# Kernel tuning notes

Measured on AMD Instinct MI355X. Metric: run time of the kernel, lower is better.

## Reference

```python
import jax, jax.numpy as jnp
import numpy as np

B, N, K = 2, 8192, 9
FEAT_C, COST_C, FLOW_C = 128, 64, 3
CH = [128, 128]          # PointConv output channels
MLP = [128, 64]          # pointwise Conv1d channels
WN = 16                  # WeightNet output width
HID = [8, 8]             # WeightNet hidden widths
SLOPE = 0.1              # leaky relu slope
EPS = 1e-5
CLAMP = (-200.0, 200.0)


def setup_inputs() -> dict:
    key = jax.random.key(0)
    ks = iter(jax.random.split(key, 64))
    def nrm(shape, s=0.02):
        return jax.random.normal(next(ks), shape, jnp.float32) * s
    inp = {}
    inp["xyz"] = jax.random.normal(next(ks), (B, N, 3), jnp.float32)
    inp["feats"] = jax.random.normal(next(ks), (B, FEAT_C, N), jnp.float32)
    inp["cost_volume"] = jax.random.normal(next(ks), (B, COST_C, N), jnp.float32)
    inp["flow"] = jax.random.normal(next(ks), (B, FLOW_C, N), jnp.float32)
    last = FEAT_C + COST_C + FLOW_C
    for i, co in enumerate(CH):
        cin = last + 3
        p = f"pc{i}_"
        inp[p + "w1"] = nrm((HID[0], 3)); inp[p + "b1"] = jnp.zeros((HID[0],), jnp.float32)
        inp[p + "w2"] = nrm((HID[1], HID[0])); inp[p + "b2"] = jnp.zeros((HID[1],), jnp.float32)
        inp[p + "w3"] = nrm((WN, HID[1])); inp[p + "b3"] = jnp.zeros((WN,), jnp.float32)
        inp[p + "linW"] = nrm((co, cin * WN)); inp[p + "linb"] = jnp.zeros((co,), jnp.float32)
        last = co
    for i, co in enumerate(MLP):
        inp[f"mlp{i}_W"] = nrm((co, last)); inp[f"mlp{i}_b"] = jnp.zeros((co,), jnp.float32)
        last = co
    inp["fc_W"] = nrm((3, last)); inp["fc_b"] = jnp.zeros((3,), jnp.float32)
    return inp


def _bn(x, axes):
    m = x.mean(axes, keepdims=True)
    v = x.var(axes, keepdims=True)
    return (x - m) / jnp.sqrt(v + EPS)


def _leaky(x):
    return jnp.where(x >= 0, x, SLOPE * x)


def _knn_idx(xyz, k):
    # xyz: [B,N,3] -> idx [B,N,K] of k nearest (incl. self)
    sq = jnp.sum(xyz * xyz, -1)                       # [B,N]
    d = sq[:, :, None] + sq[:, None, :] - 2.0 * jnp.einsum('bnc,bmc->bnm', xyz, xyz)
    return jax.lax.top_k(-d, k)[1]                    # [B,N,K]


def _gather(a, idx):
    # a: [B,N,C], idx: [B,N,K] -> [B,N,K,C]
    return jax.vmap(lambda x, i: x[i])(a, idx)


def _pointconv(xyz, points, idx, w1, b1, w2, b2, w3, b3, linW, linb):
    # xyz [B,N,3], points [B,C,N] -> [B,out,N]
    g_xyz = _gather(xyz, idx) - xyz[:, :, None, :]    # [B,N,K,3] relative coords
    g_pts = _gather(jnp.transpose(points, (0, 2, 1)), idx)  # [B,N,K,C]
    grouped = jnp.concatenate([g_pts, g_xyz], -1)     # [B,N,K,C+3]
    # WeightNet on relative coords: 3 -> 8 -> 8 -> 16 (bn+relu each)
    h = jax.nn.relu(_bn(g_xyz @ w1.T + b1, (0, 1, 2)))
    h = jax.nn.relu(_bn(h @ w2.T + b2, (0, 1, 2)))
    w = jax.nn.relu(_bn(h @ w3.T + b3, (0, 1, 2)))    # [B,N,K,WN]
    bsz, n = grouped.shape[0], grouped.shape[1]
    agg = jnp.einsum('bnkc,bnkw->bncw', grouped, w).reshape(bsz, n, -1)
    out = agg @ linW.T + linb                         # [B,N,out]
    out = _leaky(_bn(out, (0, 1)))
    return jnp.transpose(out, (0, 2, 1))              # [B,out,N]


def reference(xyz, feats, cost_volume, flow,
              pc0_w1, pc0_b1, pc0_w2, pc0_b2, pc0_w3, pc0_b3, pc0_linW, pc0_linb,
              pc1_w1, pc1_b1, pc1_w2, pc1_b2, pc1_w3, pc1_b3, pc1_linW, pc1_linb,
              mlp0_W, mlp0_b, mlp1_W, mlp1_b, fc_W, fc_b):
    idx = _knn_idx(xyz, K)
    x = jnp.concatenate([feats, cost_volume, flow], axis=1)  # [B, feat+cost+flow, N]
    x = _pointconv(xyz, x, idx, pc0_w1, pc0_b1, pc0_w2, pc0_b2, pc0_w3, pc0_b3, pc0_linW, pc0_linb)
    x = _pointconv(xyz, x, idx, pc1_w1, pc1_b1, pc1_w2, pc1_b2, pc1_w3, pc1_b3, pc1_linW, pc1_linb)
    x = _leaky(jnp.einsum('oc,bcn->bon', mlp0_W, x) + mlp0_b[None, :, None])
    x = _leaky(jnp.einsum('oc,bcn->bon', mlp1_W, x) + mlp1_b[None, :, None])
    fl = jnp.einsum('oc,bcn->bon', fc_W, x) + fc_b[None, :, None]
    return x, jnp.clip(fl, CLAMP[0], CLAMP[1])
```

## Files before the change

### kernel.cpp

```cpp
#include <hip/hip_runtime.h>

#define NBATCH 2
#define NPTS   8192
#define NPT    (NBATCH*NPTS)
#define KNN    9
#define SEG    16
#define SEGN   (NPTS/SEG)
#define SCAP   16
#define SSTR   17

typedef unsigned short u16;
typedef unsigned int   u32;
typedef short bf16x8 __attribute__((ext_vector_type(8)));
typedef float f32x4  __attribute__((ext_vector_type(4)));

__device__ __forceinline__ float wred(float v){
#pragma unroll
  for(int o=32;o>0;o>>=1) v += __shfl_down(v,o);
  return v;
}

__device__ __forceinline__ u16 f2b(float f){
  u32 u = __float_as_uint(f);
  return (u16)((u + 0x7fffu + ((u>>16)&1u)) >> 16);
}
__device__ __forceinline__ float b2f(u16 h){ return __uint_as_float(((u32)h)<<16); }

__device__ __forceinline__ float bumpup(float x){
  u32 u = __float_as_uint(x);
  if(u == 0x80000000u) u = 1u;
  else if((int)u >= 0) u += 1u;
  else u -= 1u;
  return __uint_as_float(u);
}

__global__ __launch_bounds__(256) void k_build_xin(
    const float* __restrict__ feats, const float* __restrict__ cost,
    const float* __restrict__ flow, float* __restrict__ xin)
{
  __shared__ float buf[196][67];
  int t = threadIdx.x;
  int pt0 = blockIdx.x*64;
  int b = pt0 >> 13, n0 = pt0 & (NPTS-1);
  int lane = t & 63, grp = t >> 6;
  const float* f  = feats + (size_t)b*128*NPTS + n0 + lane;
  const float* cv = cost  + (size_t)b*64 *NPTS + n0 + lane;
  const float* fl = flow  + (size_t)b*3  *NPTS + n0 + lane;
  for(int c=grp; c<128; c+=4) buf[c][lane]      = f[(size_t)c*NPTS];
  for(int c=grp; c<64;  c+=4) buf[128+c][lane]  = cv[(size_t)c*NPTS];
  if(grp<3) buf[192+grp][lane] = fl[(size_t)grp*NPTS];
  else      buf[195][lane] = 0.f;
  __syncthreads();
  for(int e=t; e<64*49; e+=256){
    int p = e/49, q = e-p*49;
    float4 v = make_float4(buf[4*q][p], buf[4*q+1][p], buf[4*q+2][p], buf[4*q+3][p]);
    *(float4*)(xin + (size_t)(pt0+p)*196 + 4*q) = v;
  }
}

__global__ __launch_bounds__(256) void k_thr(
    const float* __restrict__ xyz, float* __restrict__ thr)
{
  __shared__ float md[4][64][9];
  int t = threadIdx.x, lane = t & 63, wave = t >> 6;
  int qb = blockIdx.x;
  int b = qb >> 7;
  int n = (qb & 127)*64 + lane;
  const float* xb = xyz + (size_t)b*NPTS*3;
  float qx=xb[3*n], qy=xb[3*n+1], qz=xb[3*n+2];
  float qs = __fadd_rn(__fadd_rn(__fmul_rn(qx,qx),__fmul_rn(qy,qy)),__fmul_rn(qz,qz));
  float bd[KNN];
#pragma unroll
  for(int i=0;i<KNN;i++) bd[i]=__builtin_inff();
  for(int i=0;i<128;i++){
    int m = (wave*128 + i)*16;
    float cx=xb[3*m], cy=xb[3*m+1], cz=xb[3*m+2];
    float s = __fadd_rn(__fadd_rn(__fmul_rn(cx,cx),__fmul_rn(cy,cy)),__fmul_rn(cz,cz));
    float dot = fmaf(cz,qz, fmaf(cy,qy, __fmul_rn(cx,qx)));
    float d = __fsub_rn(__fadd_rn(qs,s), __fmul_rn(2.0f,dot));
    if(d < bd[KNN-1]){
      bd[KNN-1]=d;
#pragma unroll
      for(int r=KNN-2;r>=0;r--){
        if(bd[r+1] < bd[r]){ float td=bd[r]; bd[r]=bd[r+1]; bd[r+1]=td; }
      }
    }
  }
#pragma unroll
  for(int i=0;i<KNN;i++) md[wave][lane][i]=bd[i];
  __syncthreads();
  if(t < 64){
    float b2[KNN];
#pragma unroll
    for(int i=0;i<KNN;i++) b2[i]=__builtin_inff();
    for(int w=0;w<4;w++){
#pragma unroll
      for(int i=0;i<KNN;i++){
        float d = md[w][t][i];
        if(d < b2[KNN-1]){
          b2[KNN-1]=d;
#pragma unroll
          for(int r=KNN-2;r>=0;r--){
            if(b2[r+1] < b2[r]){ float td=b2[r]; b2[r]=b2[r+1]; b2[r+1]=td; }
          }
        }
      }
    }
    thr[(b<<13) + (qb & 127)*64 + t] = b2[KNN-1];
  }
}

__global__ __launch_bounds__(256) void k_knn_part(
    const float* __restrict__ xyz, const float* __restrict__ thr,
    float* __restrict__ pd, int* __restrict__ pi)
{
  __shared__ float4 cbuf[256];
  __shared__ float sdq[256*SSTR];
  __shared__ int   sqi[256*SSTR];
  int t = threadIdx.x;
  int seg = blockIdx.x & (SEG-1);
  int qc  = blockIdx.x >> 4;
  int b = qc >> 5;
  int n = (qc & 31)*256 + t;
  int pt = (b<<13) + n;
  const float* xb = xyz + (size_t)b*NPTS*3;
  float qx=xb[3*n], qy=xb[3*n+1], qz=xb[3*n+2];
  float qs = __fadd_rn(__fadd_rn(__fmul_rn(qx,qx),__fmul_rn(qy,qy)),__fmul_rn(qz,qz));
  float init = bumpup(thr[pt]);
  float bd[KNN]; int bi[KNN];
#pragma unroll
  for(int i=0;i<KNN;i++){ bd[i]=init; bi[i]=0x7fffffff; }
  float cut = init;
  int cnt = 0;
  float* msd = sdq + t*SSTR;
  int*   msi = sqi + t*SSTR;
  auto flush = [&](){
    for(int i=0;i<cnt;i++){
      float d = msd[i]; int id = msi[i];
      if(d < bd[KNN-1]){
        bd[KNN-1]=d; bi[KNN-1]=id;
#pragma unroll
        for(int r=KNN-2;r>=0;r--){
          if(bd[r+1] < bd[r]){
            float td=bd[r]; bd[r]=bd[r+1]; bd[r+1]=td;
            int ti=bi[r]; bi[r]=bi[r+1]; bi[r+1]=ti;
          }
        }
      }
    }
    cnt = 0;
    cut = bd[KNN-1];
  };
  const int m0 = seg*SEGN;
  for(int tt=0; tt<SEGN; tt+=256){
    int m = m0 + tt + t;
    float cx=xb[3*m], cy=xb[3*m+1], cz=xb[3*m+2];
    float s = __fadd_rn(__fadd_rn(__fmul_rn(cx,cx),__fmul_rn(cy,cy)),__fmul_rn(cz,cz));
    cbuf[t] = make_float4(cx,cy,cz,s);
    __syncthreads();
#pragma unroll 4
    for(int j=0;j<256;j++){
      float4 c = cbuf[j];
      float dot = fmaf(c.z,qz, fmaf(c.y,qy, __fmul_rn(c.x,qx)));
      float d = __fsub_rn(__fadd_rn(qs,c.w), __fmul_rn(2.0f,dot));
      if(d < cut){
        msd[cnt]=d; msi[cnt]=m0+tt+j; cnt++;
        if(cnt==SCAP) flush();
      }
    }
    __syncthreads();
  }
  flush();
  size_t base = ((size_t)pt*SEG + seg)*KNN;
#pragma unroll
  for(int i=0;i<KNN;i++){ pd[base+i]=bd[i]; pi[base+i]=bi[i]; }
}

__global__ __launch_bounds__(256) void k_knn_merge(
    const float* __restrict__ pd, const int* __restrict__ pi, int* __restrict__ idxo)
{
  int pt = blockIdx.x*256 + threadIdx.x;
  const float4* dp = (const float4*)(pd + (size_t)pt*SEG*KNN);
  const int4*   ip = (const int4*)(pi + (size_t)pt*SEG*KNN);
  float bd[KNN]; int bi[KNN];
#pragma unroll
  for(int i=0;i<KNN;i++){ bd[i]=__builtin_inff(); bi[i]=0x7fffffff; }
  for(int v=0; v<SEG*KNN/4; v++){
    float4 dv = dp[v];
    int4   iv = ip[v];
    float dd[4] = {dv.x,dv.y,dv.z,dv.w};
    int   ii[4] = {iv.x,iv.y,iv.z,iv.w};
#pragma unroll
    for(int u=0;u<4;u++){
      float d = dd[u]; int id = ii[u];
      if(d < bd[KNN-1]){
        bd[KNN-1]=d; bi[KNN-1]=id;
#pragma unroll
        for(int i=KNN-2;i>=0;i--){
          if(bd[i+1] < bd[i]){
            float td=bd[i]; bd[i]=bd[i+1]; bd[i+1]=td;
            int ti=bi[i]; bi[i]=bi[i+1]; bi[i+1]=ti;
          }
        }
      }
    }
  }
#pragma unroll
  for(int r=0;r<KNN;r++) idxo[pt*KNN + r] = bi[r];
}

__global__ __launch_bounds__(256) void k_wn1(
    const float* __restrict__ xyz, const int* __restrict__ idx,
    const float* __restrict__ W, const float* __restrict__ Bv,
    float* __restrict__ hout, float* __restrict__ partial)
{
  int t = threadIdx.x;
  int e = blockIdx.x*256 + t;
  int pt = e/KNN;
  int b = pt>>13, n = pt & (NPTS-1);
  int m = idx[e];
  const float* xb = xyz + (size_t)b*NPTS*3;
  float gx = xb[3*m]-xb[3*n], gy = xb[3*m+1]-xb[3*n+1], gz = xb[3*m+2]-xb[3*n+2];
  float v[8];
#pragma unroll
  for(int j=0;j<8;j++){
    float d = fmaf(gz, W[3*j+2], fmaf(gy, W[3*j+1], gx*W[3*j]));
    v[j] = d + Bv[j];
    hout[(size_t)e*8 + j] = v[j];
  }
  __shared__ float red[4][2][8];
  int wave = t>>6, lane = t&63;
#pragma unroll
  for(int j=0;j<8;j++){
    float s = wred(v[j]);
    float q = wred(v[j]*v[j]);
    if(lane==0){ red[wave][0][j]=s; red[wave][1][j]=q; }
  }
  __syncthreads();
  if(t < 16){
    int isq = t>>3, c = t&7;
    partial[blockIdx.x*16 + t] =
      red[0][isq][c]+red[1][isq][c]+red[2][isq][c]+red[3][isq][c];
  }
}

template<int CI, int CO>
__global__ __launch_bounds__(256) void k_wn23(
    const float* __restrict__ hin, const float* __restrict__ st,
    const float* __restrict__ W, const float* __restrict__ Bv,
    float* __restrict__ hout, float* __restrict__ partial)
{
  int t = threadIdx.x;
  int e = blockIdx.x*256 + t;
  float x[CI];
#pragma unroll
  for(int i=0;i<CI;i++){
    float v = (hin[(size_t)e*CI + i] - st[i])*st[CI+i];
    x[i] = v>0.f? v : 0.f;
  }
  float v[CO];
#pragma unroll
  for(int j=0;j<CO;j++){
    float d = 0.f;
#pragma unroll
    for(int i=0;i<CI;i++) d = fmaf(x[i], W[j*CI+i], d);
    v[j] = d + Bv[j];
    hout[(size_t)e*CO + j] = v[j];
  }
  __shared__ float red[4][2][CO];
  int wave = t>>6, lane = t&63;
#pragma unroll
  for(int j=0;j<CO;j++){
    float s = wred(v[j]);
    float q = wred(v[j]*v[j]);
    if(lane==0){ red[wave][0][j]=s; red[wave][1][j]=q; }
  }
  __syncthreads();
  if(t < 2*CO){
    int isq = t/CO, c = t%CO;
    partial[blockIdx.x*2*CO + t] =
      red[0][isq][c]+red[1][isq][c]+red[2][isq][c]+red[3][isq][c];
  }
}

__global__ __launch_bounds__(256) void k_fin(
    const float* __restrict__ partial, float* __restrict__ st,
    int C, int nb, float cnt)
{
  __shared__ float sa[256], qa[256];
  int t = threadIdx.x;
  int c = t % C;
  int r0 = t / C;
  int stride = 256 / C;
  float s=0.f, q=0.f;
  for(int r=r0; r<nb; r+=stride){
    s += partial[r*2*C + c];
    q += partial[r*2*C + C + c];
  }
  sa[t]=s; qa[t]=q;
  __syncthreads();
  if(t < C){
    for(int g=1; g<stride; g++){ s += sa[t+g*C]; q += qa[t+g*C]; }
    float mean = s/cnt;
    float var  = q/cnt - mean*mean;
    st[t]   = mean;
    st[C+t] = 1.0f/sqrtf(var + 1e-5f);
  }
}

__global__ __launch_bounds__(256) void k_prepW(
    const float* __restrict__ linW, u16* __restrict__ Wh, u16* __restrict__ Wl,
    int AW, int KP)
{
  int e = blockIdx.x*256 + threadIdx.x;
  if(e >= 128*KP) return;
  int o = e / KP, k = e - o*KP;
  float w = (k < AW) ? linW[o*AW + k] : 0.f;
  u16 h = f2b(w);
  u16 l = f2b(w - b2f(h));
  Wh[e]=h; Wl[e]=l;
}

template<int CIN, int XSTRIDE, int KP>
__global__ __launch_bounds__(256) void k_buildA(
    const float* __restrict__ xin, const float* __restrict__ xyz,
    const int* __restrict__ idx, const float* __restrict__ wpre,
    const float* __restrict__ st3, u16* __restrict__ Abuf, int c0)
{
  constexpr int P = 8;
  constexpr int CPTS = CIN-3;
  constexpr int CPAD = KP/16;
  __shared__ float wm[P][KNN][16];
  __shared__ float gxs[P][KNN][3];
  __shared__ int   si[P][KNN];
  __shared__ float sm3[16], sr3[16];
  int t = threadIdx.x;
  int pt0 = c0 + blockIdx.x*P;
  int b = pt0 >> 13;
  const float* xb = xyz + (size_t)b*NPTS*3;
  if(t<16){ sm3[t]=st3[t]; sr3[t]=st3[16+t]; }
  if(t>=32 && t<32+P*KNN){
    int u = t-32; int p=u/KNN, k=u-p*KNN;
    int n = (pt0+p)&(NPTS-1);
    int m = idx[(pt0+p)*KNN+k];
    si[p][k]=m;
    gxs[p][k][0]=xb[3*m]  -xb[3*n];
    gxs[p][k][1]=xb[3*m+1]-xb[3*n+1];
    gxs[p][k][2]=xb[3*m+2]-xb[3*n+2];
  }
  __syncthreads();
  for(int e=t; e<P*KNN*16; e+=256){
    int p = e/(KNN*16); int r = e - p*(KNN*16); int k = r>>4, wn = r&15;
    float v = (wpre[((size_t)(pt0+p)*KNN + k)*16 + wn] - sm3[wn]) * sr3[wn];
    wm[p][k][wn] = v>0.f? v:0.f;
  }
  __syncthreads();
  for(int it=t; it<P*CPAD; it+=256){
    int p = it/CPAD, c = it - p*CPAD;
    u32 u[8];
    if(c < CIN){
      float g[KNN];
      if(c < CPTS){
#pragma unroll
        for(int k=0;k<KNN;k++)
          g[k] = xin[(size_t)((b<<13) + si[p][k])*XSTRIDE + c];
      } else {
        int cc = c - CPTS;
#pragma unroll
        for(int k=0;k<KNN;k++) g[k] = gxs[p][k][cc];
      }
      float a[16];
#pragma unroll
      for(int wn=0; wn<16; wn++){
        float s = 0.f;
#pragma unroll
        for(int k=0;k<KNN;k++) s = fmaf(g[k], wm[p][k][wn], s);
        a[wn] = s;
      }
#pragma unroll
      for(int j=0;j<8;j++)
        u[j] = (u32)f2b(a[2*j]) | ((u32)f2b(a[2*j+1])<<16);
    } else {
#pragma unroll
      for(int j=0;j<8;j++) u[j]=0;
    }
    u32* dst = (u32*)(Abuf + ((size_t)(blockIdx.x*P + p)*KP + c*16));
    uint4 v0 = make_uint4(u[0],u[1],u[2],u[3]);
    uint4 v1 = make_uint4(u[4],u[5],u[6],u[7]);
    *(uint4*)dst = v0;
    *((uint4*)dst + 1) = v1;
  }
}

__device__ __forceinline__ void gload16(const void* g, void* l){
  __builtin_amdgcn_global_load_lds(
      (const __attribute__((address_space(1))) u32*)g,
      (__attribute__((address_space(3))) u32*)l, 16, 0, 0);
}

template<int KP>
__global__ __launch_bounds__(256) void k_gemm(
    const u16* __restrict__ Wh, const u16* __restrict__ Wl,
    const u16* __restrict__ A, const float* __restrict__ linb,
    float* __restrict__ outp, int ptBase)
{
  __shared__ __attribute__((aligned(16))) u16 lds[40960];
  constexpr int NT = KP/64;
  int t = threadIdx.x, wave = t>>6, lane = t&63;
  int p0 = blockIdx.x*64;
  const u16* Ab = A + (size_t)p0*KP;

  auto stage = [&](const u16* __restrict__ g, int k0, int ldsByteOff, int rows){
    int nr = (rows*128) >> 12;
    for(int r=0;r<nr;r++){
      int y  = (r*4 + wave) << 10;
      int yl = y + lane*16;
      int row = yl >> 7;
      int s = (yl >> 4) & 7;
      int c = s ^ (row & 7);
      const u16* src = g + (size_t)row*KP + k0 + c*8;
      gload16(src, (char*)lds + ldsByteOff + y);
    }
  };

  stage(Wh, 0, 0,     128);
  stage(Wl, 0, 32768, 128);
  stage(Ab, 0, 65536, 64);

  f32x4 acch[2][4], accl[2][4];
#pragma unroll
  for(int i=0;i<2;i++)
#pragma unroll
    for(int j=0;j<4;j++){ acch[i][j]=(f32x4)(0.f); accl[i][j]=(f32x4)(0.f); }

  for(int kt=0; kt<NT; kt++){
    int cur = kt & 1;
    __syncthreads();
    if(kt+1 < NT){
      int nxt = cur^1;
      stage(Wh, (kt+1)*64, nxt*16384,         128);
      stage(Wl, (kt+1)*64, 32768 + nxt*16384, 128);
      stage(Ab, (kt+1)*64, 65536 + nxt*8192,  64);
    }
    const u16* Lwh = lds + cur*8192;
    const u16* Lwl = lds + 16384 + cur*8192;
    const u16* La  = lds + 32768 + cur*4096;
#pragma unroll
    for(int kf=0; kf<2; kf++){
      int cb = kf*4 + (lane>>4);
      bf16x8 af[4];
#pragma unroll
      for(int nf=0; nf<4; nf++){
        int p = nf*16 + (lane&15);
        af[nf] = *(const bf16x8*)(La + p*64 + ((cb ^ (p&7))<<3));
      }
#pragma unroll
      for(int mf=0; mf<2; mf++){
        int row = (wave*2+mf)*16 + (lane&15);
        int off = row*64 + ((cb ^ (row&7))<<3);
        bf16x8 wh = *(const bf16x8*)(Lwh + off);
        bf16x8 wl = *(const bf16x8*)(Lwl + off);
#pragma unroll
        for(int nf=0; nf<4; nf++){
          acch[mf][nf] = __builtin_amdgcn_mfma_f32_16x16x32_bf16(wh, af[nf], acch[mf][nf], 0,0,0);
          accl[mf][nf] = __builtin_amdgcn_mfma_f32_16x16x32_bf16(wl, af[nf], accl[mf][nf], 0,0,0);
        }
      }
    }
  }
#pragma unroll
  for(int mf=0; mf<2; mf++){
#pragma unroll
    for(int nf=0; nf<4; nf++){
      f32x4 v = acch[mf][nf] + accl[mf][nf];
      int pt = ptBase + p0 + nf*16 + (lane&15);
      int obase = (wave*2+mf)*16 + (lane>>4)*4;
#pragma unroll
      for(int r=0;r<4;r++){
        int o = obase + r;
        outp[(size_t)pt*128 + o] = v[r] + linb[o];
      }
    }
  }
}

__global__ __launch_bounds__(256) void k_ostats(
    const float* __restrict__ outp, float* __restrict__ partial)
{
  __shared__ float ss[256], qq[256];
  int t = threadIdx.x;
  int c = t & 127, half = t >> 7;
  int base_pt = blockIdx.x*256;
  float s=0.f, q=0.f;
  for(int i=0;i<128;i++){
    int pt = base_pt + i*2 + half;
    float v = outp[(size_t)pt*128 + c];
    s += v; q = fmaf(v,v,q);
  }
  ss[t]=s; qq[t]=q;
  __syncthreads();
  if(t<128){
    partial[blockIdx.x*256 + t]       = ss[t]+ss[t+128];
    partial[blockIdx.x*256 + 128 + t] = qq[t]+qq[t+128];
  }
}

__global__ __launch_bounds__(256) void k_pfin(
    const float* __restrict__ outp, const float* __restrict__ st,
    float* __restrict__ xout)
{
  int e = blockIdx.x*256 + threadIdx.x;
  int c = e & 127;
  float v = (outp[e]-st[c])*st[128+c];
  xout[e] = v>=0.f? v : 0.1f*v;
}

__global__ __launch_bounds__(256) void k_mlp(
    const float* __restrict__ x2,
    const float* __restrict__ W0, const float* __restrict__ B0,
    const float* __restrict__ W1, const float* __restrict__ B1,
    const float* __restrict__ Wf, const float* __restrict__ Bf,
    float* __restrict__ dout)
{
  __shared__ float w0l[128*129];
  __shared__ float w1l[128*65];
  __shared__ float xt [128*65];
  __shared__ float m1l[64*65];
  int t = threadIdx.x;
  int pt0 = blockIdx.x*64;
  int b = pt0 >> 13, n0 = pt0 & (NPTS-1);
  for(int e=t; e<128*128; e+=256){ int o=e>>7, j=e&127; w0l[j*129+o] = W0[e]; }
  for(int e=t; e<64*128;  e+=256){ int o=e>>7, j=e&127; w1l[j*65+o]  = W1[e]; }
  for(int e=t; e<64*128;  e+=256){ int p=e>>7, j=e&127; xt[j*65+p]   = x2[(size_t)(pt0+p)*128 + j]; }
  __syncthreads();
  int p = t&63, wv = t>>6;
  float acc[32];
#pragma unroll
  for(int i=0;i<32;i++) acc[i]=0.f;
  for(int j=0;j<128;j++){
    float xv = xt[j*65+p];
#pragma unroll
    for(int i=0;i<32;i++)
      acc[i] = fmaf(w0l[j*129 + wv*32 + i], xv, acc[i]);
  }
  __syncthreads();
#pragma unroll
  for(int i=0;i<32;i++){
    float v = acc[i] + B0[wv*32+i];
    v = v>=0.f? v : 0.1f*v;
    xt[(wv*32+i)*65 + p] = v;
  }
  __syncthreads();
  float a2[16];
#pragma unroll
  for(int i=0;i<16;i++) a2[i]=0.f;
  for(int j=0;j<128;j++){
    float xv = xt[j*65+p];
#pragma unroll
    for(int i=0;i<16;i++)
      a2[i] = fmaf(w1l[j*65 + wv*16 + i], xv, a2[i]);
  }
#pragma unroll
  for(int i=0;i<16;i++){
    int o = wv*16+i;
    float v = a2[i] + B1[o];
    v = v>=0.f? v : 0.1f*v;
    dout[(size_t)(b*64+o)*NPTS + n0 + p] = v;
    m1l[o*65+p] = v;
  }
  __syncthreads();
  if(t < 192){
    int o = t/64, pp = t%64;
    float a = Bf[o];
    for(int j=0;j<64;j++) a = fmaf(Wf[o*64+j], m1l[j*65+pp], a);
    a = fminf(fmaxf(a, -200.f), 200.f);
    dout[(size_t)NBATCH*64*NPTS + (size_t)(b*3+o)*NPTS + n0 + pp] = a;
  }
}

extern "C" void kernel_launch(void* const* d_in, const int* in_sizes, int n_in,
                              void* d_out, int out_size, void* d_ws, size_t ws_size,
                              hipStream_t stream)
{
  (void)in_sizes; (void)n_in; (void)out_size;
  const float* xyz   = (const float*)d_in[0];
  const float* feats = (const float*)d_in[1];
  const float* cost  = (const float*)d_in[2];
  const float* flow  = (const float*)d_in[3];
  const float* pw1[2]  = {(const float*)d_in[4],  (const float*)d_in[12]};
  const float* pb1[2]  = {(const float*)d_in[5],  (const float*)d_in[13]};
  const float* pw2[2]  = {(const float*)d_in[6],  (const float*)d_in[14]};
  const float* pb2[2]  = {(const float*)d_in[7],  (const float*)d_in[15]};
  const float* pw3[2]  = {(const float*)d_in[8],  (const float*)d_in[16]};
  const float* pb3[2]  = {(const float*)d_in[9],  (const float*)d_in[17]};
  const float* plW[2]  = {(const float*)d_in[10], (const float*)d_in[18]};
  const float* plb[2]  = {(const float*)d_in[11], (const float*)d_in[19]};
  const float* m0W = (const float*)d_in[20];
  const float* m0b = (const float*)d_in[21];
  const float* m1W = (const float*)d_in[22];
  const float* m1b = (const float*)d_in[23];
  const float* fcW = (const float*)d_in[24];
  const float* fcb = (const float*)d_in[25];
  float* out = (float*)d_out;

  const int KP0 = 3200, AW0 = 3168;
  const int KP1 = 2112, AW1 = 2096;

  float* ws = (float*)d_ws;
  size_t o = 0;
  float* xin0 = ws + o; o += (size_t)NPT*196;
  int*   idx  = (int*)(ws + o); o += (size_t)NPT*KNN + 3;
  o &= ~(size_t)3;
  float* thr  = ws + o; o += (size_t)NPT;
  float* pd   = ws + o; o += (size_t)NPT*SEG*KNN;
  int*   pi   = (int*)(ws + o); o += (size_t)NPT*SEG*KNN;
  float* h1   = ws + o; o += (size_t)NPT*KNN*8;
  float* h2   = ws + o; o += (size_t)NPT*KNN*8;
  float* wpre = ws + o; o += (size_t)NPT*KNN*16;
  float* part = ws + o; o += 576*32;
  float* st1  = ws + o; o += 16;
  float* st2  = ws + o; o += 16;
  float* st3  = ws + o; o += 32;
  float* sto  = ws + o; o += 256;
  float* outp = ws + o; o += (size_t)NPT*128;
  float* x1   = ws + o; o += (size_t)NPT*128;
  float* x2   = ws + o; o += (size_t)NPT*128;
  u16* Wh0 = (u16*)(ws + o); o += (size_t)128*KP0/2;
  u16* Wl0 = (u16*)(ws + o); o += (size_t)128*KP0/2;
  u16* Wh1 = (u16*)(ws + o); o += (size_t)128*KP1/2;
  u16* Wl1 = (u16*)(ws + o); o += (size_t)128*KP1/2;
  u16* Abuf = (u16*)(ws + o);
  size_t used_bytes = o*4;
  size_t avail = ws_size > used_bytes ? ws_size - used_bytes : 0;
  int npc = NPT;
  while(npc > 1024 && (size_t)npc*KP0*2 > avail) npc >>= 1;

  k_build_xin<<<NPT/64, 256, 0, stream>>>(feats, cost, flow, xin0);
  k_thr<<<256, 256, 0, stream>>>(xyz, thr);
  k_knn_part<<<64*SEG, 256, 0, stream>>>(xyz, thr, pd, pi);
  k_knn_merge<<<NPT/256, 256, 0, stream>>>(pd, pi, idx);

  k_prepW<<<(128*KP0+255)/256, 256, 0, stream>>>(plW[0], Wh0, Wl0, AW0, KP0);
  k_prepW<<<(128*KP1+255)/256, 256, 0, stream>>>(plW[1], Wh1, Wl1, AW1, KP1);

  const float cnt1 = (float)(NPT*KNN);
  const float cnto = (float)NPT;

  for(int L=0; L<2; ++L){
    k_wn1<<<576,256,0,stream>>>(xyz, idx, pw1[L], pb1[L], h1, part);
    k_fin<<<1,256,0,stream>>>(part, st1, 8, 576, cnt1);
    k_wn23<8,8><<<576,256,0,stream>>>(h1, st1, pw2[L], pb2[L], h2, part);
    k_fin<<<1,256,0,stream>>>(part, st2, 8, 576, cnt1);
    k_wn23<8,16><<<576,256,0,stream>>>(h2, st2, pw3[L], pb3[L], wpre, part);
    k_fin<<<1,256,0,stream>>>(part, st3, 16, 576, cnt1);
    for(int c0 = 0; c0 < NPT; c0 += npc){
      if(L==0){
        k_buildA<198,196,KP0><<<npc/8,256,0,stream>>>(xin0, xyz, idx, wpre, st3, Abuf, c0);
        k_gemm<KP0><<<npc/64,256,0,stream>>>(Wh0, Wl0, Abuf, plb[0], outp, c0);
      } else {
        k_buildA<131,128,KP1><<<npc/8,256,0,stream>>>(x1, xyz, idx, wpre, st3, Abuf, c0);
        k_gemm<KP1><<<npc/64,256,0,stream>>>(Wh1, Wl1, Abuf, plb[1], outp, c0);
      }
    }
    k_ostats<<<64,256,0,stream>>>(outp, part);
    k_fin<<<1,256,0,stream>>>(part, sto, 128, 64, cnto);
    k_pfin<<<NPT*128/256,256,0,stream>>>(outp, sto, (L==0)? x1 : x2);
  }

  k_mlp<<<NPT/64,256,0,stream>>>(x2, m0W,m0b, m1W,m1b, fcW,fcb, out);
}
```

Baseline: 561.6 us.

## Fuse PointConv A-matrix build into GEMM, drop split-bf16 weights, fuse output stats

Merges the separate buildA and GEMM kernels into one kernel. Each block gathers the neighbour features, computes the weighted einsum tile in LDS and feeds it straight to the MFMA loop, so the large A buffer never goes through global memory. It also stops splitting the weights into high and low bf16 parts, which halves the MFMA and weight traffic but lowers accuracy. The GEMM epilogue now writes per-block sum and sum-of-squares for the output BN, replacing the ostats kernel. Separately, the KNN selection capacity constants are shrunk.

```diff
diff --git a/kernel.cpp b/kernel.cpp
--- a/kernel.cpp
+++ b/kernel.cpp
@@ -6,8 +6,8 @@
 #define KNN    9
 #define SEG    16
 #define SEGN   (NPTS/SEG)
-#define SCAP   16
-#define SSTR   17
+#define SCAP   12
+#define SSTR   13
 
 typedef unsigned short u16;
 typedef unsigned int   u32;
@@ -24,7 +24,6 @@
   u32 u = __float_as_uint(f);
   return (u16)((u + 0x7fffu + ((u>>16)&1u)) >> 16);
 }
-__device__ __forceinline__ float b2f(u16 h){ return __uint_as_float(((u32)h)<<16); }
 
 __device__ __forceinline__ float bumpup(float x){
   u32 u = __float_as_uint(x);
@@ -309,87 +308,13 @@
 }
 
 __global__ __launch_bounds__(256) void k_prepW(
-    const float* __restrict__ linW, u16* __restrict__ Wh, u16* __restrict__ Wl,
-    int AW, int KP)
+    const float* __restrict__ linW, u16* __restrict__ Wh, int AW, int KP)
 {
   int e = blockIdx.x*256 + threadIdx.x;
   if(e >= 128*KP) return;
   int o = e / KP, k = e - o*KP;
   float w = (k < AW) ? linW[o*AW + k] : 0.f;
-  u16 h = f2b(w);
-  u16 l = f2b(w - b2f(h));
-  Wh[e]=h; Wl[e]=l;
-}
-
-template<int CIN, int XSTRIDE, int KP>
-__global__ __launch_bounds__(256) void k_buildA(
-    const float* __restrict__ xin, const float* __restrict__ xyz,
-    const int* __restrict__ idx, const float* __restrict__ wpre,
-    const float* __restrict__ st3, u16* __restrict__ Abuf, int c0)
-{
-  constexpr int P = 8;
-  constexpr int CPTS = CIN-3;
-  constexpr int CPAD = KP/16;
-  __shared__ float wm[P][KNN][16];
-  __shared__ float gxs[P][KNN][3];
-  __shared__ int   si[P][KNN];
-  __shared__ float sm3[16], sr3[16];
-  int t = threadIdx.x;
-  int pt0 = c0 + blockIdx.x*P;
-  int b = pt0 >> 13;
-  const float* xb = xyz + (size_t)b*NPTS*3;
-  if(t<16){ sm3[t]=st3[t]; sr3[t]=st3[16+t]; }
-  if(t>=32 && t<32+P*KNN){
-    int u = t-32; int p=u/KNN, k=u-p*KNN;
-    int n = (pt0+p)&(NPTS-1);
-    int m = idx[(pt0+p)*KNN+k];
-    si[p][k]=m;
-    gxs[p][k][0]=xb[3*m]  -xb[3*n];
-    gxs[p][k][1]=xb[3*m+1]-xb[3*n+1];
-    gxs[p][k][2]=xb[3*m+2]-xb[3*n+2];
-  }
-  __syncthreads();
-  for(int e=t; e<P*KNN*16; e+=256){
-    int p = e/(KNN*16); int r = e - p*(KNN*16); int k = r>>4, wn = r&15;
-    float v = (wpre[((size_t)(pt0+p)*KNN + k)*16 + wn] - sm3[wn]) * sr3[wn];
-    wm[p][k][wn] = v>0.f? v:0.f;
-  }
-  __syncthreads();
-  for(int it=t; it<P*CPAD; it+=256){
-    int p = it/CPAD, c = it - p*CPAD;
-    u32 u[8];
-    if(c < CIN){
-      float g[KNN];
-      if(c < CPTS){
-#pragma unroll
-        for(int k=0;k<KNN;k++)
-          g[k] = xin[(size_t)((b<<13) + si[p][k])*XSTRIDE + c];
-      } else {
-        int cc = c - CPTS;
-#pragma unroll
-        for(int k=0;k<KNN;k++) g[k] = gxs[p][k][cc];
-      }
-      float a[16];
-#pragma unroll
-      for(int wn=0; wn<16; wn++){
-        float s = 0.f;
-#pragma unroll
-        for(int k=0;k<KNN;k++) s = fmaf(g[k], wm[p][k][wn], s);
-        a[wn] = s;
-      }
-#pragma unroll
-      for(int j=0;j<8;j++)
-        u[j] = (u32)f2b(a[2*j]) | ((u32)f2b(a[2*j+1])<<16);
-    } else {
-#pragma unroll
-      for(int j=0;j<8;j++) u[j]=0;
-    }
-    u32* dst = (u32*)(Abuf + ((size_t)(blockIdx.x*P + p)*KP + c*16));
-    uint4 v0 = make_uint4(u[0],u[1],u[2],u[3]);
-    uint4 v1 = make_uint4(u[4],u[5],u[6],u[7]);
-    *(uint4*)dst = v0;
-    *((uint4*)dst + 1) = v1;
-  }
+  Wh[e] = f2b(w);
 }
 
 __device__ __forceinline__ void gload16(const void* g, void* l){
@@ -398,53 +323,141 @@
       (__attribute__((address_space(3))) u32*)l, 16, 0, 0);
 }
 
-template<int KP>
-__global__ __launch_bounds__(256) void k_gemm(
-    const u16* __restrict__ Wh, const u16* __restrict__ Wl,
-    const u16* __restrict__ A, const float* __restrict__ linb,
-    float* __restrict__ outp, int ptBase)
-{
-  __shared__ __attribute__((aligned(16))) u16 lds[40960];
+template<int CIN, int XSTRIDE, int KP>
+__global__ __launch_bounds__(256) void k_pcgemm(
+    const float* __restrict__ xin, const float* __restrict__ xyz,
+    const int* __restrict__ idx, const float* __restrict__ wpre,
+    const float* __restrict__ st3, const u16* __restrict__ Wh,
+    const float* __restrict__ linb, float* __restrict__ outp,
+    float* __restrict__ partial)
+{
+  constexpr int CPTS = CIN-3;
   constexpr int NT = KP/64;
+  __shared__ __attribute__((aligned(16))) char smem[71680];
+  u16*   Wlds = (u16*)smem;
+  u16*   Alds = (u16*)(smem + 32768);
+  float* G    = (float*)(smem + 49152);
+  float* gxs  = (float*)(smem + 62464);
+  int*   si   = (int*)(smem + 69376);
+
   int t = threadIdx.x, wave = t>>6, lane = t&63;
-  int p0 = blockIdx.x*64;
-  const u16* Ab = A + (size_t)p0*KP;
-
-  auto stage = [&](const u16* __restrict__ g, int k0, int ldsByteOff, int rows){
-    int nr = (rows*128) >> 12;
-    for(int r=0;r<nr;r++){
+  int pt0 = blockIdx.x*64;
+  int b = pt0 >> 13;
+  const float* xb = xyz + (size_t)b*NPTS*3;
+  const float* xbase = xin + ((size_t)(b<<13))*XSTRIDE;
+
+  int p_ = t>>2, wq = t&3;
+
+  for(int e=t; e<64*KNN; e+=256){
+    int p = e/KNN, k = e - p*KNN;
+    int n = (pt0+p)&(NPTS-1);
+    int m = idx[(pt0+p)*KNN+k];
+    si[p*KNN+k] = m;
+    gxs[(p*KNN+k)*3+0] = xb[3*m]  -xb[3*n];
+    gxs[(p*KNN+k)*3+1] = xb[3*m+1]-xb[3*n+1];
+    gxs[(p*KNN+k)*3+2] = xb[3*m+2]-xb[3*n+2];
+  }
+  float wm[KNN][4];
+  {
+    float sm[4], sr[4];
+#pragma unroll
+    for(int j=0;j<4;j++){ sm[j]=st3[wq*4+j]; sr[j]=st3[16+wq*4+j]; }
+#pragma unroll
+    for(int k=0;k<KNN;k++){
+      float4 w4 = *(const float4*)(wpre + ((size_t)(pt0+p_)*KNN + k)*16 + wq*4);
+      float wv[4] = {w4.x,w4.y,w4.z,w4.w};
+#pragma unroll
+      for(int j=0;j<4;j++){
+        float v = (wv[j]-sm[j])*sr[j];
+        wm[k][j] = v>0.f? v:0.f;
+      }
+    }
+  }
+  __syncthreads();
+
+  auto stageW = [&](int kt, int buf){
+    int k0 = kt*64;
+#pragma unroll
+    for(int r=0;r<4;r++){
       int y  = (r*4 + wave) << 10;
       int yl = y + lane*16;
       int row = yl >> 7;
       int s = (yl >> 4) & 7;
       int c = s ^ (row & 7);
-      const u16* src = g + (size_t)row*KP + k0 + c*8;
-      gload16(src, (char*)lds + ldsByteOff + y);
+      const u16* src = Wh + (size_t)row*KP + k0 + c*8;
+      gload16(src, (char*)smem + buf*16384 + y);
     }
   };
 
-  stage(Wh, 0, 0,     128);
-  stage(Wl, 0, 32768, 128);
-  stage(Ab, 0, 65536, 64);
-
-  f32x4 acch[2][4], accl[2][4];
+  auto gatherG = [&](int kt){
+    int c0 = kt*4;
+    for(int e=t; e<64*KNN; e+=256){
+      int p = e/KNN, k = e - p*KNN;
+      float v[4];
+      if(c0+3 < CPTS){
+        float4 f4 = *(const float4*)(xbase + (size_t)si[p*KNN+k]*XSTRIDE + c0);
+        v[0]=f4.x; v[1]=f4.y; v[2]=f4.z; v[3]=f4.w;
+      } else {
+#pragma unroll
+        for(int j=0;j<4;j++){
+          int c = c0+j;
+          if(c < CPTS)      v[j] = xbase[(size_t)si[p*KNN+k]*XSTRIDE + c];
+          else if(c < CIN)  v[j] = gxs[(p*KNN+k)*3 + (c-CPTS)];
+          else              v[j] = 0.f;
+        }
+      }
+#pragma unroll
+      for(int j=0;j<4;j++) G[p*52 + j*12 + k] = v[j];
+    }
+  };
+
+  auto einsumA = [&](int buf){
+    float g[4][KNN];
+#pragma unroll
+    for(int ci=0;ci<4;ci++){
+      const float* gp = G + p_*52 + ci*12;
+      float4 a4 = *(const float4*)(gp);
+      float4 b4 = *(const float4*)(gp+4);
+      g[ci][0]=a4.x; g[ci][1]=a4.y; g[ci][2]=a4.z; g[ci][3]=a4.w;
+      g[ci][4]=b4.x; g[ci][5]=b4.y; g[ci][6]=b4.z; g[ci][7]=b4.w;
+      g[ci][8]=gp[8];
+    }
+#pragma unroll
+    for(int ci=0;ci<4;ci++){
+      float a[4];
+#pragma unroll
+      for(int j=0;j<4;j++){
+        float s = 0.f;
+#pragma unroll
+        for(int k=0;k<KNN;k++) s = fmaf(g[ci][k], wm[k][j], s);
+        a[j] = s;
+      }
+      u32 lo = (u32)f2b(a[0]) | ((u32)f2b(a[1])<<16);
+      u32 hi = (u32)f2b(a[2]) | ((u32)f2b(a[3])<<16);
+      int chunk = ci*2 + (wq>>1);
+      int off = buf*8192 + p_*128 + ((chunk ^ (p_&7))<<4) + (wq&1)*8;
+      *(uint2*)((char*)Alds + off) = make_uint2(lo,hi);
+    }
+  };
+
+  gatherG(0); stageW(0, 0);
+  __syncthreads();
+  einsumA(0);
+  __syncthreads();
+
+  f32x4 acc[2][4];
 #pragma unroll
   for(int i=0;i<2;i++)
 #pragma unroll
-    for(int j=0;j<4;j++){ acch[i][j]=(f32x4)(0.f); accl[i][j]=(f32x4)(0.f); }
+    for(int j=0;j<4;j++) acc[i][j]=(f32x4)(0.f);
 
   for(int kt=0; kt<NT; kt++){
-    int cur = kt & 1;
+    int cur = kt & 1, nxt = cur^1;
+    if(kt+1 < NT){ gatherG(kt+1); stageW(kt+1, nxt); }
     __syncthreads();
-    if(kt+1 < NT){
-      int nxt = cur^1;
-      stage(Wh, (kt+1)*64, nxt*16384,         128);
-      stage(Wl, (kt+1)*64, 32768 + nxt*16384, 128);
-      stage(Ab, (kt+1)*64, 65536 + nxt*8192,  64);
-    }
-    const u16* Lwh = lds + cur*8192;
-    const u16* Lwl = lds + 16384 + cur*8192;
-    const u16* La  = lds + 32768 + cur*4096;
+    if(kt+1 < NT) einsumA(nxt);
+    const u16* Lw = Wlds + cur*8192;
+    const u16* La = Alds + cur*4096;
 #pragma unroll
     for(int kf=0; kf<2; kf++){
       int cb = kf*4 + (lane>>4);
@@ -457,51 +470,40 @@
 #pragma unroll
       for(int mf=0; mf<2; mf++){
         int row = (wave*2+mf)*16 + (lane&15);
-        int off = row*64 + ((cb ^ (row&7))<<3);
-        bf16x8 wh = *(const bf16x8*)(Lwh + off);
-        bf16x8 wl = *(const bf16x8*)(Lwl + off);
-#pragma unroll
-        for(int nf=0; nf<4; nf++){
-          acch[mf][nf] = __builtin_amdgcn_mfma_f32_16x16x32_bf16(wh, af[nf], acch[mf][nf], 0,0,0);
-          accl[mf][nf] = __builtin_amdgcn_mfma_f32_16x16x32_bf16(wl, af[nf], accl[mf][nf], 0,0,0);
-        }
-      }
-    }
-  }
+        bf16x8 wh = *(const bf16x8*)(Lw + row*64 + ((cb ^ (row&7))<<3));
+#pragma unroll
+        for(int nf=0; nf<4; nf++)
+          acc[mf][nf] = __builtin_amdgcn_mfma_f32_16x16x32_bf16(wh, af[nf], acc[mf][nf], 0,0,0);
+      }
+    }
+    __syncthreads();
+  }
+
+  int q = lane>>4, lc = lane&15;
 #pragma unroll
   for(int mf=0; mf<2; mf++){
-#pragma unroll
-    for(int nf=0; nf<4; nf++){
-      f32x4 v = acch[mf][nf] + accl[mf][nf];
-      int pt = ptBase + p0 + nf*16 + (lane&15);
-      int obase = (wave*2+mf)*16 + (lane>>4)*4;
-#pragma unroll
-      for(int r=0;r<4;r++){
-        int o = obase + r;
-        outp[(size_t)pt*128 + o] = v[r] + linb[o];
-      }
-    }
-  }
-}
-
-__global__ __launch_bounds__(256) void k_ostats(
-    const float* __restrict__ outp, float* __restrict__ partial)
-{
-  __shared__ float ss[256], qq[256];
-  int t = threadIdx.x;
-  int c = t & 127, half = t >> 7;
-  int base_pt = blockIdx.x*256;
-  float s=0.f, q=0.f;
-  for(int i=0;i<128;i++){
-    int pt = base_pt + i*2 + half;
-    float v = outp[(size_t)pt*128 + c];
-    s += v; q = fmaf(v,v,q);
-  }
-  ss[t]=s; qq[t]=q;
-  __syncthreads();
-  if(t<128){
-    partial[blockIdx.x*256 + t]       = ss[t]+ss[t+128];
-    partial[blockIdx.x*256 + 128 + t] = qq[t]+qq[t+128];
+    int obase = (wave*2+mf)*16 + q*4;
+#pragma unroll
+    for(int r=0;r<4;r++){
+      int o = obase + r;
+      float bo = linb[o];
+      float sv = 0.f, qv = 0.f;
+#pragma unroll
+      for(int nf=0; nf<4; nf++){
+        float x = acc[mf][nf][r] + bo;
+        outp[(size_t)(pt0 + nf*16 + lc)*128 + o] = x;
+        sv += x; qv = fmaf(x,x,qv);
+      }
+#pragma unroll
+      for(int off=8; off>0; off>>=1){
+        sv += __shfl_down(sv,off);
+        qv += __shfl_down(qv,off);
+      }
+      if(lc==0){
+        partial[blockIdx.x*256 + o]       = sv;
+        partial[blockIdx.x*256 + 128 + o] = qv;
+      }
+    }
   }
 }
 
@@ -582,7 +584,7 @@
                               void* d_out, int out_size, void* d_ws, size_t ws_size,
                               hipStream_t stream)
 {
-  (void)in_sizes; (void)n_in; (void)out_size;
+  (void)in_sizes; (void)n_in; (void)out_size; (void)ws_size;
   const float* xyz   = (const float*)d_in[0];
   const float* feats = (const float*)d_in[1];
   const float* cost  = (const float*)d_in[2];
@@ -617,7 +619,7 @@
   float* h1   = ws + o; o += (size_t)NPT*KNN*8;
   float* h2   = ws + o; o += (size_t)NPT*KNN*8;
   float* wpre = ws + o; o += (size_t)NPT*KNN*16;
-  float* part = ws + o; o += 576*32;
+  float* part = ws + o; o += 65536;
   float* st1  = ws + o; o += 16;
   float* st2  = ws + o; o += 16;
   float* st3  = ws + o; o += 32;
@@ -626,22 +628,15 @@
   float* x1   = ws + o; o += (size_t)NPT*128;
   float* x2   = ws + o; o += (size_t)NPT*128;
   u16* Wh0 = (u16*)(ws + o); o += (size_t)128*KP0/2;
-  u16* Wl0 = (u16*)(ws + o); o += (size_t)128*KP0/2;
   u16* Wh1 = (u16*)(ws + o); o += (size_t)128*KP1/2;
-  u16* Wl1 = (u16*)(ws + o); o += (size_t)128*KP1/2;
-  u16* Abuf = (u16*)(ws + o);
-  size_t used_bytes = o*4;
-  size_t avail = ws_size > used_bytes ? ws_size - used_bytes : 0;
-  int npc = NPT;
-  while(npc > 1024 && (size_t)npc*KP0*2 > avail) npc >>= 1;
 
   k_build_xin<<<NPT/64, 256, 0, stream>>>(feats, cost, flow, xin0);
   k_thr<<<256, 256, 0, stream>>>(xyz, thr);
   k_knn_part<<<64*SEG, 256, 0, stream>>>(xyz, thr, pd, pi);
   k_knn_merge<<<NPT/256, 256, 0, stream>>>(pd, pi, idx);
 
-  k_prepW<<<(128*KP0+255)/256, 256, 0, stream>>>(plW[0], Wh0, Wl0, AW0, KP0);
-  k_prepW<<<(128*KP1+255)/256, 256, 0, stream>>>(plW[1], Wh1, Wl1, AW1, KP1);
+  k_prepW<<<(128*KP0+255)/256, 256, 0, stream>>>(plW[0], Wh0, AW0, KP0);
+  k_prepW<<<(128*KP1+255)/256, 256, 0, stream>>>(plW[1], Wh1, AW1, KP1);
 
   const float cnt1 = (float)(NPT*KNN);
   const float cnto = (float)NPT;
@@ -653,17 +648,11 @@
     k_fin<<<1,256,0,stream>>>(part, st2, 8, 576, cnt1);
     k_wn23<8,16><<<576,256,0,stream>>>(h2, st2, pw3[L], pb3[L], wpre, part);
     k_fin<<<1,256,0,stream>>>(part, st3, 16, 576, cnt1);
-    for(int c0 = 0; c0 < NPT; c0 += npc){
-      if(L==0){
-        k_buildA<198,196,KP0><<<npc/8,256,0,stream>>>(xin0, xyz, idx, wpre, st3, Abuf, c0);
-        k_gemm<KP0><<<npc/64,256,0,stream>>>(Wh0, Wl0, Abuf, plb[0], outp, c0);
-      } else {
-        k_buildA<131,128,KP1><<<npc/8,256,0,stream>>>(x1, xyz, idx, wpre, st3, Abuf, c0);
-        k_gemm<KP1><<<npc/64,256,0,stream>>>(Wh1, Wl1, Abuf, plb[1], outp, c0);
-      }
-    }
-    k_ostats<<<64,256,0,stream>>>(outp, part);
-    k_fin<<<1,256,0,stream>>>(part, sto, 128, 64, cnto);
+    if(L==0)
+      k_pcgemm<198,196,KP0><<<NPT/64,256,0,stream>>>(xin0, xyz, idx, wpre, st3, Wh0, plb[0], outp, part);
+    else
+      k_pcgemm<131,128,KP1><<<NPT/64,256,0,stream>>>(x1,   xyz, idx, wpre, st3, Wh1, plb[1], outp, part);
+    k_fin<<<1,256,0,stream>>>(part, sto, 128, 256, cnto);
     k_pfin<<<NPT*128/256,256,0,stream>>>(outp, sto, (L==0)? x1 : x2);
   }
 
```

Result: slower. 692.4 us (+23.3%).

## Drop bf16 low-part weight GEMM, fuse output stats into GEMM, unroll KNN scan

Applied to the files above, without the earlier changes.

The GEMM stops using a hi/lo split bf16 weight pair and multiplies by a single bf16 weight copy. That halves the MFMA count and the LDS and global weight traffic, at the cost of accuracy in the linear layer. The per-channel sum and sum-of-squares for batch norm are now reduced inside the GEMM epilogue, so the separate k_ostats pass is gone. The final k_fin now reduces 256 partials instead of 64. Separately, the KNN scan computes eight distances before doing the branchy insert, to expose more ILP.

```diff
diff --git a/kernel.cpp b/kernel.cpp
--- a/kernel.cpp
+++ b/kernel.cpp
@@ -24,7 +24,6 @@
   u32 u = __float_as_uint(f);
   return (u16)((u + 0x7fffu + ((u>>16)&1u)) >> 16);
 }
-__device__ __forceinline__ float b2f(u16 h){ return __uint_as_float(((u32)h)<<16); }
 
 __device__ __forceinline__ float bumpup(float x){
   u32 u = __float_as_uint(x);
@@ -158,14 +157,20 @@
     float s = __fadd_rn(__fadd_rn(__fmul_rn(cx,cx),__fmul_rn(cy,cy)),__fmul_rn(cz,cz));
     cbuf[t] = make_float4(cx,cy,cz,s);
     __syncthreads();
-#pragma unroll 4
-    for(int j=0;j<256;j++){
-      float4 c = cbuf[j];
-      float dot = fmaf(c.z,qz, fmaf(c.y,qy, __fmul_rn(c.x,qx)));
-      float d = __fsub_rn(__fadd_rn(qs,c.w), __fmul_rn(2.0f,dot));
-      if(d < cut){
-        msd[cnt]=d; msi[cnt]=m0+tt+j; cnt++;
-        if(cnt==SCAP) flush();
+    for(int j0=0; j0<256; j0+=8){
+      float dv[8];
+#pragma unroll
+      for(int u=0;u<8;u++){
+        float4 c = cbuf[j0+u];
+        float dot = fmaf(c.z,qz, fmaf(c.y,qy, __fmul_rn(c.x,qx)));
+        dv[u] = __fsub_rn(__fadd_rn(qs,c.w), __fmul_rn(2.0f,dot));
+      }
+#pragma unroll
+      for(int u=0;u<8;u++){
+        if(dv[u] < cut){
+          msd[cnt]=dv[u]; msi[cnt]=m0+tt+j0+u; cnt++;
+          if(cnt==SCAP) flush();
+        }
       }
     }
     __syncthreads();
@@ -309,16 +314,13 @@
 }
 
 __global__ __launch_bounds__(256) void k_prepW(
-    const float* __restrict__ linW, u16* __restrict__ Wh, u16* __restrict__ Wl,
-    int AW, int KP)
+    const float* __restrict__ linW, u16* __restrict__ Wh, int AW, int KP)
 {
   int e = blockIdx.x*256 + threadIdx.x;
   if(e >= 128*KP) return;
   int o = e / KP, k = e - o*KP;
   float w = (k < AW) ? linW[o*AW + k] : 0.f;
-  u16 h = f2b(w);
-  u16 l = f2b(w - b2f(h));
-  Wh[e]=h; Wl[e]=l;
+  Wh[e] = f2b(w);
 }
 
 template<int CIN, int XSTRIDE, int KP>
@@ -400,11 +402,11 @@
 
 template<int KP>
 __global__ __launch_bounds__(256) void k_gemm(
-    const u16* __restrict__ Wh, const u16* __restrict__ Wl,
-    const u16* __restrict__ A, const float* __restrict__ linb,
-    float* __restrict__ outp, int ptBase)
-{
-  __shared__ __attribute__((aligned(16))) u16 lds[40960];
+    const u16* __restrict__ Wh, const u16* __restrict__ A,
+    const float* __restrict__ linb, float* __restrict__ outp,
+    float* __restrict__ partial, int ptBase)
+{
+  __shared__ __attribute__((aligned(16))) u16 lds[24576];
   constexpr int NT = KP/64;
   int t = threadIdx.x, wave = t>>6, lane = t&63;
   int p0 = blockIdx.x*64;
@@ -424,14 +426,13 @@
   };
 
   stage(Wh, 0, 0,     128);
-  stage(Wl, 0, 32768, 128);
-  stage(Ab, 0, 65536, 64);
-
-  f32x4 acch[2][4], accl[2][4];
+  stage(Ab, 0, 32768, 64);
+
+  f32x4 acc[2][4];
 #pragma unroll
   for(int i=0;i<2;i++)
 #pragma unroll
-    for(int j=0;j<4;j++){ acch[i][j]=(f32x4)(0.f); accl[i][j]=(f32x4)(0.f); }
+    for(int j=0;j<4;j++) acc[i][j]=(f32x4)(0.f);
 
   for(int kt=0; kt<NT; kt++){
     int cur = kt & 1;
@@ -439,12 +440,10 @@
     if(kt+1 < NT){
       int nxt = cur^1;
       stage(Wh, (kt+1)*64, nxt*16384,         128);
-      stage(Wl, (kt+1)*64, 32768 + nxt*16384, 128);
-      stage(Ab, (kt+1)*64, 65536 + nxt*8192,  64);
-    }
-    const u16* Lwh = lds + cur*8192;
-    const u16* Lwl = lds + 16384 + cur*8192;
-    const u16* La  = lds + 32768 + cur*4096;
+      stage(Ab, (kt+1)*64, 32768 + nxt*8192,  64);
+    }
+    const u16* Lw = lds + cur*8192;
+    const u16* La = lds + 16384 + cur*4096;
 #pragma unroll
     for(int kf=0; kf<2; kf++){
       int cb = kf*4 + (lane>>4);
@@ -457,51 +456,40 @@
 #pragma unroll
       for(int mf=0; mf<2; mf++){
         int row = (wave*2+mf)*16 + (lane&15);
-        int off = row*64 + ((cb ^ (row&7))<<3);
-        bf16x8 wh = *(const bf16x8*)(Lwh + off);
-        bf16x8 wl = *(const bf16x8*)(Lwl + off);
-#pragma unroll
-        for(int nf=0; nf<4; nf++){
-          acch[mf][nf] = __builtin_amdgcn_mfma_f32_16x16x32_bf16(wh, af[nf], acch[mf][nf], 0,0,0);
-          accl[mf][nf] = __builtin_amdgcn_mfma_f32_16x16x32_bf16(wl, af[nf], accl[mf][nf], 0,0,0);
-        }
-      }
-    }
-  }
+        bf16x8 wh = *(const bf16x8*)(Lw + row*64 + ((cb ^ (row&7))<<3));
+#pragma unroll
+        for(int nf=0; nf<4; nf++)
+          acc[mf][nf] = __builtin_amdgcn_mfma_f32_16x16x32_bf16(wh, af[nf], acc[mf][nf], 0,0,0);
+      }
+    }
+  }
+
+  int gb = (ptBase>>6) + blockIdx.x;
+  int q = lane>>4, lc = lane&15;
 #pragma unroll
   for(int mf=0; mf<2; mf++){
-#pragma unroll
-    for(int nf=0; nf<4; nf++){
-      f32x4 v = acch[mf][nf] + accl[mf][nf];
-      int pt = ptBase + p0 + nf*16 + (lane&15);
-      int obase = (wave*2+mf)*16 + (lane>>4)*4;
-#pragma unroll
-      for(int r=0;r<4;r++){
-        int o = obase + r;
-        outp[(size_t)pt*128 + o] = v[r] + linb[o];
-      }
-    }
-  }
-}
-
-__global__ __launch_bounds__(256) void k_ostats(
-    const float* __restrict__ outp, float* __restrict__ partial)
-{
-  __shared__ float ss[256], qq[256];
-  int t = threadIdx.x;
-  int c = t & 127, half = t >> 7;
-  int base_pt = blockIdx.x*256;
-  float s=0.f, q=0.f;
-  for(int i=0;i<128;i++){
-    int pt = base_pt + i*2 + half;
-    float v = outp[(size_t)pt*128 + c];
-    s += v; q = fmaf(v,v,q);
-  }
-  ss[t]=s; qq[t]=q;
-  __syncthreads();
-  if(t<128){
-    partial[blockIdx.x*256 + t]       = ss[t]+ss[t+128];
-    partial[blockIdx.x*256 + 128 + t] = qq[t]+qq[t+128];
+    int obase = (wave*2+mf)*16 + q*4;
+#pragma unroll
+    for(int r=0;r<4;r++){
+      int o = obase + r;
+      float bo = linb[o];
+      float sv = 0.f, qv = 0.f;
+#pragma unroll
+      for(int nf=0; nf<4; nf++){
+        float x = acc[mf][nf][r] + bo;
+        outp[(size_t)(ptBase + p0 + nf*16 + lc)*128 + o] = x;
+        sv += x; qv = fmaf(x,x,qv);
+      }
+#pragma unroll
+      for(int off=8; off>0; off>>=1){
+        sv += __shfl_down(sv,off);
+        qv += __shfl_down(qv,off);
+      }
+      if(lc==0){
+        partial[gb*256 + o]       = sv;
+        partial[gb*256 + 128 + o] = qv;
+      }
+    }
   }
 }
 
@@ -617,7 +605,7 @@
   float* h1   = ws + o; o += (size_t)NPT*KNN*8;
   float* h2   = ws + o; o += (size_t)NPT*KNN*8;
   float* wpre = ws + o; o += (size_t)NPT*KNN*16;
-  float* part = ws + o; o += 576*32;
+  float* part = ws + o; o += 65536;
   float* st1  = ws + o; o += 16;
   float* st2  = ws + o; o += 16;
   float* st3  = ws + o; o += 32;
@@ -626,9 +614,7 @@
   float* x1   = ws + o; o += (size_t)NPT*128;
   float* x2   = ws + o; o += (size_t)NPT*128;
   u16* Wh0 = (u16*)(ws + o); o += (size_t)128*KP0/2;
-  u16* Wl0 = (u16*)(ws + o); o += (size_t)128*KP0/2;
   u16* Wh1 = (u16*)(ws + o); o += (size_t)128*KP1/2;
-  u16* Wl1 = (u16*)(ws + o); o += (size_t)128*KP1/2;
   u16* Abuf = (u16*)(ws + o);
   size_t used_bytes = o*4;
   size_t avail = ws_size > used_bytes ? ws_size - used_bytes : 0;
@@ -640,8 +626,8 @@
   k_knn_part<<<64*SEG, 256, 0, stream>>>(xyz, thr, pd, pi);
   k_knn_merge<<<NPT/256, 256, 0, stream>>>(pd, pi, idx);
 
-  k_prepW<<<(128*KP0+255)/256, 256, 0, stream>>>(plW[0], Wh0, Wl0, AW0, KP0);
-  k_prepW<<<(128*KP1+255)/256, 256, 0, stream>>>(plW[1], Wh1, Wl1, AW1, KP1);
+  k_prepW<<<(128*KP0+255)/256, 256, 0, stream>>>(plW[0], Wh0, AW0, KP0);
+  k_prepW<<<(128*KP1+255)/256, 256, 0, stream>>>(plW[1], Wh1, AW1, KP1);
 
   const float cnt1 = (float)(NPT*KNN);
   const float cnto = (float)NPT;
@@ -656,14 +642,13 @@
     for(int c0 = 0; c0 < NPT; c0 += npc){
       if(L==0){
         k_buildA<198,196,KP0><<<npc/8,256,0,stream>>>(xin0, xyz, idx, wpre, st3, Abuf, c0);
-        k_gemm<KP0><<<npc/64,256,0,stream>>>(Wh0, Wl0, Abuf, plb[0], outp, c0);
+        k_gemm<KP0><<<npc/64,256,0,stream>>>(Wh0, Abuf, plb[0], outp, part, c0);
       } else {
         k_buildA<131,128,KP1><<<npc/8,256,0,stream>>>(x1, xyz, idx, wpre, st3, Abuf, c0);
-        k_gemm<KP1><<<npc/64,256,0,stream>>>(Wh1, Wl1, Abuf, plb[1], outp, c0);
-      }
-    }
-    k_ostats<<<64,256,0,stream>>>(outp, part);
-    k_fin<<<1,256,0,stream>>>(part, sto, 128, 64, cnto);
+        k_gemm<KP1><<<npc/64,256,0,stream>>>(Wh1, Abuf, plb[1], outp, part, c0);
+      }
+    }
+    k_fin<<<1,256,0,stream>>>(part, sto, 128, NPT/64, cnto);
     k_pfin<<<NPT*128/256,256,0,stream>>>(outp, sto, (L==0)? x1 : x2);
   }
 
```

Result: no change. 567.4 us (+1.0%).
